# Performance work log

Measured on AMD Instinct MI355X. Metric: run time of the kernel, lower is better.

## Reference

```python
import jax, jax.numpy as jnp
import numpy as np

B, T, E, H = 2, 2048, 1024, 16
D = E // H  # head_dim = 64


def setup_inputs() -> dict:
    key = jax.random.key(0)
    ks = jax.random.split(key, 7)
    s = 1.0 / np.sqrt(E)
    queries = jax.random.normal(ks[0], (B, T, E), dtype=jnp.float32)
    keys = jax.random.normal(ks[1], (B, T, E), dtype=jnp.float32)
    values = jax.random.normal(ks[2], (B, T, E), dtype=jnp.float32)
    # causal mask: True where attention is disallowed (masked_fill semantics)
    mask = jnp.triu(jnp.ones((T, T), dtype=bool), k=1)[None, None]  # [1,1,T,T]
    Wq = jax.random.uniform(ks[3], (E, E), jnp.float32, -s, s)
    Wk = jax.random.uniform(ks[4], (E, E), jnp.float32, -s, s)
    Wv = jax.random.uniform(ks[5], (E, E), jnp.float32, -s, s)
    Wo = jax.random.uniform(ks[6], (E, E), jnp.float32, -s, s)
    return {"queries": queries, "keys": keys, "values": values, "mask": mask,
            "Wq": Wq, "Wk": Wk, "Wv": Wv, "Wo": Wo}


def _split(x):
    # [B,T,E] -> [B,H,T,D]
    return x.reshape(B, T, H, D).transpose(0, 2, 1, 3)


def reference(queries, keys, values, mask, Wq, Wk, Wv, Wo):
    # nn.Linear(E,E,bias=False): y = x @ W.T
    q = _split(queries @ Wq.T)  # [B,H,T,D]
    k = _split(keys @ Wk.T)
    v = _split(values @ Wv.T)
    scores = jnp.einsum('bhqd,bhkd->bhqk', q, k) / jnp.sqrt(jnp.float32(D))
    scores = jnp.where(mask, -jnp.inf, scores)
    weights = jax.nn.softmax(scores, axis=-1)
    attn = jnp.einsum('bhqk,bhkd->bhqd', weights, v)  # [B,H,T,D]
    joined = attn.transpose(0, 2, 1, 3).reshape(B, T, E)
    return joined @ Wo.T
```

## Files before the change

kernel.cpp:

```cpp
#include <hip/hip_runtime.h>
#include <hip/hip_bf16.h>

#define T_DIM 2048
#define E_DIM 1024
#define MM 4096
#define NN 1024
#define KK 1024
#define MSZ ((size_t)MM * KK)
#define WSZ ((size_t)NN * KK)

typedef __attribute__((ext_vector_type(8))) short bh8;
typedef __attribute__((ext_vector_type(4))) short bh4;
typedef __attribute__((ext_vector_type(4))) float fx4;

static __device__ __forceinline__ short f2bf(float f) {
  union { float f; unsigned u; } v; v.f = f;
  unsigned r = (v.u + 0x7fffu + ((v.u >> 16) & 1u)) >> 16;
  return (short)(unsigned short)r;
}

static __device__ __forceinline__ void gload16(const void* g, void* l) {
  __builtin_amdgcn_global_load_lds(
      (const __attribute__((address_space(1))) unsigned*)g,
      (__attribute__((address_space(3))) unsigned*)l, 16, 0, 0);
}

template<int CTRL>
static __device__ __forceinline__ float dppf(float x) {
  union { float f; int i; } a, b;
  a.f = x;
  b.i = __builtin_amdgcn_update_dpp(0, a.i, CTRL, 0xf, 0xf, false);
  return b.f;
}
static __device__ __forceinline__ float rowmax16(float x) {
  x = fmaxf(x, dppf<0x121>(x));
  x = fmaxf(x, dppf<0x122>(x));
  x = fmaxf(x, dppf<0x124>(x));
  x = fmaxf(x, dppf<0x128>(x));
  return x;
}
static __device__ __forceinline__ float rowsum16(float x) {
  x += dppf<0x121>(x);
  x += dppf<0x122>(x);
  x += dppf<0x124>(x);
  x += dppf<0x128>(x);
  return x;
}

__global__ __launch_bounds__(256) void cvt_w(const float* __restrict__ s0,
                                             const float* __restrict__ s1,
                                             const float* __restrict__ s2,
                                             const float* __restrict__ s3,
                                             short* __restrict__ dst) {
  int a = blockIdx.y;
  const float* sp = a == 0 ? s0 : a == 1 ? s1 : a == 2 ? s2 : s3;
  size_t i = ((size_t)blockIdx.x * 256 + threadIdx.x) * 8;
  fx4 x = *(const fx4*)(sp + i);
  fx4 y = *(const fx4*)(sp + i + 4);
  bh8 o;
#pragma unroll
  for (int j = 0; j < 4; j++) { o[j] = f2bf(x[j]); o[4 + j] = f2bf(y[j]); }
  *(bh8*)(dst + (size_t)a * WSZ + i) = o;
}

__global__ __launch_bounds__(256) void cvt_act(const float* __restrict__ s0,
                                               const float* __restrict__ s1,
                                               const float* __restrict__ s2,
                                               short* __restrict__ dst) {
  int a = blockIdx.y;
  const float* sp = a == 0 ? s0 : a == 1 ? s1 : s2;
  size_t i = ((size_t)blockIdx.x * 256 + threadIdx.x) * 8;
  fx4 x = *(const fx4*)(sp + i);
  fx4 y = *(const fx4*)(sp + i + 4);
  bh8 o;
#pragma unroll
  for (int j = 0; j < 4; j++) { o[j] = f2bf(x[j]); o[4 + j] = f2bf(y[j]); }
  *(bh8*)(dst + (size_t)a * MSZ + i) = o;
}

template<bool AF32, bool OUTF32>
__global__ __launch_bounds__(256) void gemm_fast(const void* __restrict__ A0,
                                                 const void* __restrict__ A1,
                                                 const void* __restrict__ A2,
                                                 const short* __restrict__ W0,
                                                 void* __restrict__ C0)
{
  __shared__ short As[128 * 32];
  __shared__ short Bs[128 * 32];
  const int tid = threadIdx.x;
  const int lane = tid & 63, w = tid >> 6;
  const int lm = lane & 15, lg = lane >> 4;
  const int wr = w >> 1, wc = w & 1;
  const int m0 = blockIdx.y * 128, n0 = blockIdx.x * 128;
  const int z = blockIdx.z;
  const void* Ap = z == 0 ? A0 : z == 1 ? A1 : A2;
  const short* W = W0 + (size_t)z * WSZ;

  fx4 acc[4][4] = {};

  for (int k0 = 0; k0 < KK; k0 += 32) {
    __syncthreads();
#pragma unroll
    for (int c = 0; c < 2; c++) {
      int idx = c * 256 + tid;
      int row = idx >> 2, kc = idx & 3;
      gload16(W + (size_t)(n0 + row) * KK + k0 + kc * 8, Bs + idx * 8);
      if constexpr (AF32) {
        const float* Af = (const float*)Ap;
        const float* src = Af + (size_t)(m0 + row) * KK + k0 + kc * 8;
        fx4 x = *(const fx4*)src;
        fx4 y = *(const fx4*)(src + 4);
        bh8 o;
#pragma unroll
        for (int j = 0; j < 4; j++) { o[j] = f2bf(x[j]); o[4 + j] = f2bf(y[j]); }
        *(bh8*)&As[idx * 8] = o;
      } else {
        const short* Ab = (const short*)Ap;
        gload16(Ab + (size_t)(m0 + row) * KK + k0 + kc * 8, As + idx * 8);
      }
    }
    __syncthreads();
    bh8 af[4], bf[4];
#pragma unroll
    for (int mi = 0; mi < 4; mi++)
      af[mi] = *(const bh8*)&As[(wr * 64 + mi * 16 + lm) * 32 + lg * 8];
#pragma unroll
    for (int ni = 0; ni < 4; ni++)
      bf[ni] = *(const bh8*)&Bs[(wc * 64 + ni * 16 + lm) * 32 + lg * 8];
#pragma unroll
    for (int mi = 0; mi < 4; mi++)
#pragma unroll
      for (int ni = 0; ni < 4; ni++)
        acc[mi][ni] = __builtin_amdgcn_mfma_f32_16x16x32_bf16(af[mi], bf[ni], acc[mi][ni], 0, 0, 0);
  }

#pragma unroll
  for (int mi = 0; mi < 4; mi++)
#pragma unroll
    for (int ni = 0; ni < 4; ni++) {
      int row = m0 + wr * 64 + mi * 16 + lg * 4;
      int col = n0 + wc * 64 + ni * 16 + lm;
#pragma unroll
      for (int r = 0; r < 4; r++) {
        float vv = acc[mi][ni][r];
        if constexpr (OUTF32) ((float*)C0)[(size_t)z * MSZ + (size_t)(row + r) * NN + col] = vv;
        else ((short*)C0)[(size_t)z * MSZ + (size_t)(row + r) * NN + col] = f2bf(vv);
      }
    }
}

__global__ __launch_bounds__(256) void gemm_out64(const short* __restrict__ A,
                                                  const short* __restrict__ W,
                                                  float* __restrict__ C)
{
  __shared__ short As[64 * 32];
  __shared__ short Bs[128 * 32];
  const int tid = threadIdx.x;
  const int lane = tid & 63, w = tid >> 6;
  const int lm = lane & 15, lg = lane >> 4;
  const int lin = blockIdx.x + 8 * blockIdx.y;
  const int swz = (lin & 7) * 64 + (lin >> 3);
  const int n0 = (swz & 7) * 128, m0 = (swz >> 3) * 64;

  fx4 acc[4][2] = {};

  for (int k0 = 0; k0 < KK; k0 += 32) {
    __syncthreads();
    {
      int row = tid >> 2, kc = tid & 3;
      gload16(A + (size_t)(m0 + row) * KK + k0 + kc * 8, As + tid * 8);
#pragma unroll
      for (int c = 0; c < 2; c++) {
        int idx = c * 256 + tid;
        int brow = idx >> 2, bkc = idx & 3;
        gload16(W + (size_t)(n0 + brow) * KK + k0 + bkc * 8, Bs + idx * 8);
      }
    }
    __syncthreads();
    bh8 af[4], bf[2];
#pragma unroll
    for (int mi = 0; mi < 4; mi++)
      af[mi] = *(const bh8*)&As[(mi * 16 + lm) * 32 + lg * 8];
#pragma unroll
    for (int ni = 0; ni < 2; ni++)
      bf[ni] = *(const bh8*)&Bs[(w * 32 + ni * 16 + lm) * 32 + lg * 8];
#pragma unroll
    for (int mi = 0; mi < 4; mi++)
#pragma unroll
      for (int ni = 0; ni < 2; ni++)
        acc[mi][ni] = __builtin_amdgcn_mfma_f32_16x16x32_bf16(af[mi], bf[ni], acc[mi][ni], 0, 0, 0);
  }

#pragma unroll
  for (int mi = 0; mi < 4; mi++)
#pragma unroll
    for (int ni = 0; ni < 2; ni++) {
      int row = m0 + mi * 16 + lg * 4;
      int col = n0 + w * 32 + ni * 16 + lm;
#pragma unroll
      for (int r = 0; r < 4; r++)
        C[(size_t)(row + r) * NN + col] = acc[mi][ni][r];
    }
}

template<bool AF32, bool OUTF32>
__global__ __launch_bounds__(256) void gemm_nt(const void* __restrict__ Ap,
                                               const float* __restrict__ Bw,
                                               void* __restrict__ Cp,
                                               int M, int N, int K)
{
  __shared__ short As[128 * 40];
  __shared__ short Bs[128 * 40];
  const int tid = threadIdx.x;
  const int lane = tid & 63;
  const int w = tid >> 6;
  const int lm = lane & 15;
  const int lg = lane >> 4;
  const int wr = w >> 1, wc = w & 1;
  const int m0 = blockIdx.y * 128, n0 = blockIdx.x * 128;

  fx4 acc[4][4] = {};

  for (int k0 = 0; k0 < K; k0 += 32) {
    __syncthreads();
#pragma unroll
    for (int i = 0; i < 4; ++i) {
      int g = i * 256 + tid;
      int row = g >> 3, cg = g & 7;
      bh4 a4;
      if constexpr (AF32) {
        const float* A = (const float*)Ap;
        fx4 v = *(const fx4*)(A + (size_t)(m0 + row) * K + k0 + cg * 4);
#pragma unroll
        for (int j = 0; j < 4; j++) a4[j] = f2bf(v[j]);
      } else {
        const short* A = (const short*)Ap;
        a4 = *(const bh4*)(A + (size_t)(m0 + row) * K + k0 + cg * 4);
      }
      *(bh4*)&As[row * 40 + cg * 4] = a4;

      fx4 bv = *(const fx4*)(Bw + (size_t)(n0 + row) * K + k0 + cg * 4);
      bh4 b4;
#pragma unroll
      for (int j = 0; j < 4; j++) b4[j] = f2bf(bv[j]);
      *(bh4*)&Bs[row * 40 + cg * 4] = b4;
    }
    __syncthreads();

    bh8 af[4], bf[4];
#pragma unroll
    for (int mi = 0; mi < 4; mi++)
      af[mi] = *(const bh8*)&As[(wr * 64 + mi * 16 + lm) * 40 + lg * 8];
#pragma unroll
    for (int ni = 0; ni < 4; ni++)
      bf[ni] = *(const bh8*)&Bs[(wc * 64 + ni * 16 + lm) * 40 + lg * 8];
#pragma unroll
    for (int mi = 0; mi < 4; mi++)
#pragma unroll
      for (int ni = 0; ni < 4; ni++)
        acc[mi][ni] = __builtin_amdgcn_mfma_f32_16x16x32_bf16(af[mi], bf[ni], acc[mi][ni], 0, 0, 0);
  }

#pragma unroll
  for (int mi = 0; mi < 4; mi++) {
#pragma unroll
    for (int ni = 0; ni < 4; ni++) {
      int row = m0 + wr * 64 + mi * 16 + lg * 4;
      int col = n0 + wc * 64 + ni * 16 + lm;
#pragma unroll
      for (int r = 0; r < 4; r++) {
        float vv = acc[mi][ni][r];
        if constexpr (OUTF32) ((float*)Cp)[(size_t)(row + r) * N + col] = vv;
        else        ((short*)Cp)[(size_t)(row + r) * N + col] = f2bf(vv);
      }
    }
  }
}

__global__ __launch_bounds__(256) void attn_kernel(const short* __restrict__ Q,
                                                   const short* __restrict__ Kb,
                                                   const short* __restrict__ Vb,
                                                   short* __restrict__ At)
{
  __shared__ short Kl[2][64 * 64];
  __shared__ short Vt[2][64 * 64];
  __shared__ short Pl[4 * 16 * 72];

  const int tid = threadIdx.x;
  const int lane = tid & 63;
  const int w = tid >> 6;
  const int lm = lane & 15;
  const int lg = lane >> 4;
  const int lin = blockIdx.x + 16 * blockIdx.y;
  const int swz = (lin & 7) * 64 + (lin >> 3);
  const int pi = swz & 15;
  const int bh = swz >> 4;
  const size_t headoff = (size_t)(bh >> 4) * T_DIM * E_DIM + (size_t)(bh & 15) * 64;

  const float SCALE2 = 0.125f * 1.44269504f;

  const int r0 = tid >> 3, ch0 = tid & 7;
  const int r1 = (256 + tid) >> 3, ch1 = tid & 7;

  for (int s = 0; s < 2; s++) {
    const int qt = s ? (31 - pi) : pi;
    const int q0 = qt * 64;

    const int qrow = q0 + w * 16 + lm;
    bh8 qf[2];
#pragma unroll
    for (int ks = 0; ks < 2; ks++)
      qf[ks] = *(const bh8*)(Q + headoff + (size_t)qrow * E_DIM + ks * 32 + lg * 8);

    fx4 oacc[4] = {};
    float m_r[4], l_r[4];
#pragma unroll
    for (int r = 0; r < 4; r++) { m_r[r] = -INFINITY; l_r[r] = 0.0f; }

    {
      gload16(Kb + headoff + (size_t)r0 * E_DIM + ((ch0 ^ (r0 & 7)) * 8), &Kl[0][tid * 8]);
      gload16(Kb + headoff + (size_t)r1 * E_DIM + ((ch1 ^ (r1 & 7)) * 8), &Kl[0][(256 + tid) * 8]);
      bh8 v8a = *(const bh8*)(Vb + headoff + (size_t)r0 * E_DIM + ch0 * 8);
      bh8 v8b = *(const bh8*)(Vb + headoff + (size_t)r1 * E_DIM + ch1 * 8);
#pragma unroll
      for (int j = 0; j < 8; j++) {
        int d = ch0 * 8 + j;
        Vt[0][d * 64 + (((r0 >> 3) ^ ((ch0 + j) & 7)) * 8) + (r0 & 7)] = v8a[j];
        Vt[0][d * 64 + (((r1 >> 3) ^ ((ch1 + j) & 7)) * 8) + (r1 & 7)] = v8b[j];
      }
    }
    __syncthreads();

    int cur = 0;
    for (int t = 0; t <= qt; ++t) {
      const bool pre = (t < qt);
      bh8 v8a, v8b;
      if (pre) {
        const int kvn = (t + 1) * 64;
        gload16(Kb + headoff + (size_t)(kvn + r0) * E_DIM + ((ch0 ^ (r0 & 7)) * 8),
                &Kl[cur ^ 1][tid * 8]);
        gload16(Kb + headoff + (size_t)(kvn + r1) * E_DIM + ((ch1 ^ (r1 & 7)) * 8),
                &Kl[cur ^ 1][(256 + tid) * 8]);
        v8a = *(const bh8*)(Vb + headoff + (size_t)(kvn + r0) * E_DIM + ch0 * 8);
        v8b = *(const bh8*)(Vb + headoff + (size_t)(kvn + r1) * E_DIM + ch1 * 8);
      }

      fx4 sacc[4] = {};
#pragma unroll
      for (int nb = 0; nb < 4; nb++) {
        const int rK = nb * 16 + lm;
#pragma unroll
        for (int ks = 0; ks < 2; ks++) {
          bh8 kf = *(const bh8*)&Kl[cur][rK * 64 + (((ks * 4 + lg) ^ (lm & 7)) * 8)];
          sacc[nb] = __builtin_amdgcn_mfma_f32_16x16x32_bf16(qf[ks], kf, sacc[nb], 0, 0, 0);
        }
      }

      float sv[4][4];
      const bool maskt = (t == qt);
#pragma unroll
      for (int nb = 0; nb < 4; nb++)
#pragma unroll
        for (int r = 0; r < 4; r++) {
          float x = sacc[nb][r] * SCALE2;
          if (maskt && (nb * 16 + lm > w * 16 + lg * 4 + r)) x = -INFINITY;
          sv[nb][r] = x;
        }

      float p[4][4];
#pragma unroll
      for (int r = 0; r < 4; r++) {
        float rm = fmaxf(fmaxf(sv[0][r], sv[1][r]), fmaxf(sv[2][r], sv[3][r]));
        rm = rowmax16(rm);
        float mn = fmaxf(m_r[r], rm);
        float fac = exp2f(m_r[r] - mn);
        float ps = 0.0f;
#pragma unroll
        for (int nb = 0; nb < 4; nb++) { p[nb][r] = exp2f(sv[nb][r] - mn); ps += p[nb][r]; }
        ps = rowsum16(ps);
        l_r[r] = l_r[r] * fac + ps;
        m_r[r] = mn;
#pragma unroll
        for (int db = 0; db < 4; db++) oacc[db][r] *= fac;
      }

#pragma unroll
      for (int nb = 0; nb < 4; nb++)
#pragma unroll
        for (int r = 0; r < 4; r++)
          Pl[w * 1152 + (lg * 4 + r) * 72 + nb * 16 + lm] = f2bf(p[nb][r]);

      bh8 pa[2];
#pragma unroll
      for (int ks = 0; ks < 2; ks++)
        pa[ks] = *(const bh8*)&Pl[w * 1152 + lm * 72 + ks * 32 + lg * 8];
#pragma unroll
      for (int db = 0; db < 4; db++) {
        const int d = db * 16 + lm;
        const int gsw = ((d >> 3) + (d & 7)) & 7;
#pragma unroll
        for (int ks = 0; ks < 2; ks++) {
          bh8 vf = *(const bh8*)&Vt[cur][d * 64 + (((ks * 4 + lg) ^ gsw) * 8)];
          oacc[db] = __builtin_amdgcn_mfma_f32_16x16x32_bf16(pa[ks], vf, oacc[db], 0, 0, 0);
        }
      }

      if (pre) {
#pragma unroll
        for (int j = 0; j < 8; j++) {
          int d = ch0 * 8 + j;
          Vt[cur ^ 1][d * 64 + (((r0 >> 3) ^ ((ch0 + j) & 7)) * 8) + (r0 & 7)] = v8a[j];
          Vt[cur ^ 1][d * 64 + (((r1 >> 3) ^ ((ch1 + j) & 7)) * 8) + (r1 & 7)] = v8b[j];
        }
      }
      __syncthreads();
      cur ^= 1;
    }

#pragma unroll
    for (int r = 0; r < 4; r++) {
      float rl = 1.0f / l_r[r];
      int row = q0 + w * 16 + lg * 4 + r;
#pragma unroll
      for (int db = 0; db < 4; db++)
        At[headoff + (size_t)row * E_DIM + db * 16 + lm] = f2bf(oacc[db][r] * rl);
    }
  }
}

extern "C" void kernel_launch(void* const* d_in, const int* in_sizes, int n_in,
                              void* d_out, int out_size, void* d_ws, size_t ws_size,
                              hipStream_t stream)
{
  const float* q  = (const float*)d_in[0];
  const float* k  = (const float*)d_in[1];
  const float* v  = (const float*)d_in[2];
  const float* Wq = (const float*)d_in[4];
  const float* Wk = (const float*)d_in[5];
  const float* Wv = (const float*)d_in[6];
  const float* Wo = (const float*)d_in[7];

  short* Qb  = (short*)d_ws;
  short* Kbb = Qb + MSZ;
  short* Vbb = Kbb + MSZ;
  short* wqb = Vbb + MSZ;
  short* Xq  = wqb + 4 * WSZ;
  short* At  = Xq;

  const size_t need_full = (3 * MSZ + 4 * WSZ + 3 * MSZ) * 2;
  const size_t need_mid  = (4 * MSZ + 4 * WSZ) * 2;

  if (ws_size >= need_full) {
    cvt_act<<<dim3(MSZ / (256 * 8), 3), 256, 0, stream>>>(q, k, v, Xq);
    cvt_w<<<dim3(WSZ / (256 * 8), 4), 256, 0, stream>>>(Wq, Wk, Wv, Wo, wqb);
    gemm_fast<false, false><<<dim3(NN / 128, MM / 128, 3), 256, 0, stream>>>(
        Xq, Xq + MSZ, Xq + 2 * MSZ, wqb, Qb);
    attn_kernel<<<dim3(16, 32), 256, 0, stream>>>(Qb, Kbb, Vbb, At);
    gemm_out64<<<dim3(NN / 128, MM / 64), 256, 0, stream>>>(
        At, wqb + 3 * WSZ, (float*)d_out);
  } else if (ws_size >= need_mid) {
    short* At2  = Vbb + MSZ;
    short* wqb2 = At2 + MSZ;
    cvt_w<<<dim3(WSZ / (256 * 8), 4), 256, 0, stream>>>(Wq, Wk, Wv, Wo, wqb2);
    gemm_fast<true, false><<<dim3(NN / 128, MM / 128, 3), 256, 0, stream>>>(q, k, v, wqb2, Qb);
    attn_kernel<<<dim3(16, 32), 256, 0, stream>>>(Qb, Kbb, Vbb, At2);
    gemm_out64<<<dim3(NN / 128, MM / 64), 256, 0, stream>>>(
        At2, wqb2 + 3 * WSZ, (float*)d_out);
  } else {
    short* At2 = Vbb + MSZ;
    dim3 gg(NN / 128, MM / 128);
    gemm_nt<true, false><<<gg, 256, 0, stream>>>(q, Wq, Qb, MM, NN, KK);
    gemm_nt<true, false><<<gg, 256, 0, stream>>>(k, Wk, Kbb, MM, NN, KK);
    gemm_nt<true, false><<<gg, 256, 0, stream>>>(v, Wv, Vbb, MM, NN, KK);
    attn_kernel<<<dim3(16, 32), 256, 0, stream>>>(Qb, Kbb, Vbb, At2);
    gemm_nt<false, true><<<gg, 256, 0, stream>>>(At2, Wo, d_out, MM, NN, KK);
  }
}
```

Measured before the change: 251.5 us.

## Fold softmax scale into Wq, use hardware bf16 pack, deepen GEMM K-step, skip rescale

Multiplies Wq by the softmax scale times log2(e) during weight conversion, so the attention kernel no longer scales scores. Float-to-bf16 rounding now uses the packed v_cvt_pk_bf16_f32 instruction instead of integer arithmetic. Both GEMMs load 64 K-elements per barrier pair instead of 32, which halves the number of sync rounds. The attention kernel skips the running-max rescale of the accumulators when no row max grew across the wave. The code path for mid-sized workspaces is removed. Rounding of Q moves slightly because the scale is now applied before the bf16 cast.

```diff
diff --git a/kernel.cpp b/kernel.cpp
--- a/kernel.cpp
+++ b/kernel.cpp
@@ -12,11 +12,19 @@
 typedef __attribute__((ext_vector_type(8))) short bh8;
 typedef __attribute__((ext_vector_type(4))) short bh4;
 typedef __attribute__((ext_vector_type(4))) float fx4;
+typedef __attribute__((ext_vector_type(4))) unsigned ux4;
+
+#define QSCALE 0.18033688f
 
 static __device__ __forceinline__ short f2bf(float f) {
-  union { float f; unsigned u; } v; v.f = f;
-  unsigned r = (v.u + 0x7fffu + ((v.u >> 16) & 1u)) >> 16;
-  return (short)(unsigned short)r;
+  unsigned o;
+  asm("v_cvt_pk_bf16_f32 %0, %1, %1" : "=v"(o) : "v"(f));
+  return (short)(o & 0xffffu);
+}
+static __device__ __forceinline__ unsigned f2bf2(float lo, float hi) {
+  unsigned o;
+  asm("v_cvt_pk_bf16_f32 %0, %1, %2" : "=v"(o) : "v"(lo), "v"(hi));
+  return o;
 }
 
 static __device__ __forceinline__ void gload16(const void* g, void* l) {
@@ -54,13 +62,16 @@
                                              short* __restrict__ dst) {
   int a = blockIdx.y;
   const float* sp = a == 0 ? s0 : a == 1 ? s1 : a == 2 ? s2 : s3;
+  const float sc = (a == 0) ? QSCALE : 1.0f;
   size_t i = ((size_t)blockIdx.x * 256 + threadIdx.x) * 8;
   fx4 x = *(const fx4*)(sp + i);
   fx4 y = *(const fx4*)(sp + i + 4);
-  bh8 o;
-#pragma unroll
-  for (int j = 0; j < 4; j++) { o[j] = f2bf(x[j]); o[4 + j] = f2bf(y[j]); }
-  *(bh8*)(dst + (size_t)a * WSZ + i) = o;
+  ux4 o;
+  o[0] = f2bf2(x[0] * sc, x[1] * sc);
+  o[1] = f2bf2(x[2] * sc, x[3] * sc);
+  o[2] = f2bf2(y[0] * sc, y[1] * sc);
+  o[3] = f2bf2(y[2] * sc, y[3] * sc);
+  *(ux4*)(dst + (size_t)a * WSZ + i) = o;
 }
 
 __global__ __launch_bounds__(256) void cvt_act(const float* __restrict__ s0,
@@ -72,66 +83,65 @@
   size_t i = ((size_t)blockIdx.x * 256 + threadIdx.x) * 8;
   fx4 x = *(const fx4*)(sp + i);
   fx4 y = *(const fx4*)(sp + i + 4);
-  bh8 o;
-#pragma unroll
-  for (int j = 0; j < 4; j++) { o[j] = f2bf(x[j]); o[4 + j] = f2bf(y[j]); }
-  *(bh8*)(dst + (size_t)a * MSZ + i) = o;
-}
-
-template<bool AF32, bool OUTF32>
-__global__ __launch_bounds__(256) void gemm_fast(const void* __restrict__ A0,
-                                                 const void* __restrict__ A1,
-                                                 const void* __restrict__ A2,
+  ux4 o;
+  o[0] = f2bf2(x[0], x[1]);
+  o[1] = f2bf2(x[2], x[3]);
+  o[2] = f2bf2(y[0], y[1]);
+  o[3] = f2bf2(y[2], y[3]);
+  *(ux4*)(dst + (size_t)a * MSZ + i) = o;
+}
+
+template<bool OUTF32>
+__global__ __launch_bounds__(256) void gemm_fast(const short* __restrict__ A0,
+                                                 const short* __restrict__ A1,
+                                                 const short* __restrict__ A2,
                                                  const short* __restrict__ W0,
                                                  void* __restrict__ C0)
 {
-  __shared__ short As[128 * 32];
-  __shared__ short Bs[128 * 32];
+  __shared__ short As[2][128 * 32];
+  __shared__ short Bs[2][128 * 32];
   const int tid = threadIdx.x;
   const int lane = tid & 63, w = tid >> 6;
   const int lm = lane & 15, lg = lane >> 4;
   const int wr = w >> 1, wc = w & 1;
   const int m0 = blockIdx.y * 128, n0 = blockIdx.x * 128;
   const int z = blockIdx.z;
-  const void* Ap = z == 0 ? A0 : z == 1 ? A1 : A2;
+  const short* Ab = z == 0 ? A0 : z == 1 ? A1 : A2;
   const short* W = W0 + (size_t)z * WSZ;
 
   fx4 acc[4][4] = {};
 
-  for (int k0 = 0; k0 < KK; k0 += 32) {
-    __syncthreads();
-#pragma unroll
-    for (int c = 0; c < 2; c++) {
-      int idx = c * 256 + tid;
-      int row = idx >> 2, kc = idx & 3;
-      gload16(W + (size_t)(n0 + row) * KK + k0 + kc * 8, Bs + idx * 8);
-      if constexpr (AF32) {
-        const float* Af = (const float*)Ap;
-        const float* src = Af + (size_t)(m0 + row) * KK + k0 + kc * 8;
-        fx4 x = *(const fx4*)src;
-        fx4 y = *(const fx4*)(src + 4);
-        bh8 o;
-#pragma unroll
-        for (int j = 0; j < 4; j++) { o[j] = f2bf(x[j]); o[4 + j] = f2bf(y[j]); }
-        *(bh8*)&As[idx * 8] = o;
-      } else {
-        const short* Ab = (const short*)Ap;
-        gload16(Ab + (size_t)(m0 + row) * KK + k0 + kc * 8, As + idx * 8);
-      }
-    }
-    __syncthreads();
-    bh8 af[4], bf[4];
+  for (int k0 = 0; k0 < KK; k0 += 64) {
+    __syncthreads();
+#pragma unroll
+    for (int h = 0; h < 2; h++) {
+#pragma unroll
+      for (int c = 0; c < 2; c++) {
+        int idx = c * 256 + tid;
+        int row = idx >> 2, kc = idx & 3;
+        gload16(W + (size_t)(n0 + row) * KK + k0 + h * 32 + kc * 8, &Bs[h][idx * 8]);
+        gload16(Ab + (size_t)(m0 + row) * KK + k0 + h * 32 + kc * 8, &As[h][idx * 8]);
+      }
+    }
+    __syncthreads();
+    bh8 af[4][2], bf[4][2];
 #pragma unroll
     for (int mi = 0; mi < 4; mi++)
-      af[mi] = *(const bh8*)&As[(wr * 64 + mi * 16 + lm) * 32 + lg * 8];
+#pragma unroll
+      for (int h = 0; h < 2; h++)
+        af[mi][h] = *(const bh8*)&As[h][(wr * 64 + mi * 16 + lm) * 32 + lg * 8];
 #pragma unroll
     for (int ni = 0; ni < 4; ni++)
-      bf[ni] = *(const bh8*)&Bs[(wc * 64 + ni * 16 + lm) * 32 + lg * 8];
+#pragma unroll
+      for (int h = 0; h < 2; h++)
+        bf[ni][h] = *(const bh8*)&Bs[h][(wc * 64 + ni * 16 + lm) * 32 + lg * 8];
 #pragma unroll
     for (int mi = 0; mi < 4; mi++)
 #pragma unroll
       for (int ni = 0; ni < 4; ni++)
-        acc[mi][ni] = __builtin_amdgcn_mfma_f32_16x16x32_bf16(af[mi], bf[ni], acc[mi][ni], 0, 0, 0);
+#pragma unroll
+        for (int h = 0; h < 2; h++)
+          acc[mi][ni] = __builtin_amdgcn_mfma_f32_16x16x32_bf16(af[mi][h], bf[ni][h], acc[mi][ni], 0, 0, 0);
   }
 
 #pragma unroll
@@ -153,8 +163,8 @@
                                                   const short* __restrict__ W,
                                                   float* __restrict__ C)
 {
-  __shared__ short As[64 * 32];
-  __shared__ short Bs[128 * 32];
+  __shared__ short As[2][64 * 32];
+  __shared__ short Bs[2][128 * 32];
   const int tid = threadIdx.x;
   const int lane = tid & 63, w = tid >> 6;
   const int lm = lane & 15, lg = lane >> 4;
@@ -164,31 +174,40 @@
 
   fx4 acc[4][2] = {};
 
-  for (int k0 = 0; k0 < KK; k0 += 32) {
-    __syncthreads();
-    {
-      int row = tid >> 2, kc = tid & 3;
-      gload16(A + (size_t)(m0 + row) * KK + k0 + kc * 8, As + tid * 8);
+  for (int k0 = 0; k0 < KK; k0 += 64) {
+    __syncthreads();
+#pragma unroll
+    for (int h = 0; h < 2; h++) {
+      {
+        int row = tid >> 2, kc = tid & 3;
+        gload16(A + (size_t)(m0 + row) * KK + k0 + h * 32 + kc * 8, &As[h][tid * 8]);
+      }
 #pragma unroll
       for (int c = 0; c < 2; c++) {
         int idx = c * 256 + tid;
         int brow = idx >> 2, bkc = idx & 3;
-        gload16(W + (size_t)(n0 + brow) * KK + k0 + bkc * 8, Bs + idx * 8);
-      }
-    }
-    __syncthreads();
-    bh8 af[4], bf[2];
+        gload16(W + (size_t)(n0 + brow) * KK + k0 + h * 32 + bkc * 8, &Bs[h][idx * 8]);
+      }
+    }
+    __syncthreads();
+    bh8 af[4][2], bf[2][2];
 #pragma unroll
     for (int mi = 0; mi < 4; mi++)
-      af[mi] = *(const bh8*)&As[(mi * 16 + lm) * 32 + lg * 8];
+#pragma unroll
+      for (int h = 0; h < 2; h++)
+        af[mi][h] = *(const bh8*)&As[h][(mi * 16 + lm) * 32 + lg * 8];
 #pragma unroll
     for (int ni = 0; ni < 2; ni++)
-      bf[ni] = *(const bh8*)&Bs[(w * 32 + ni * 16 + lm) * 32 + lg * 8];
+#pragma unroll
+      for (int h = 0; h < 2; h++)
+        bf[ni][h] = *(const bh8*)&Bs[h][(w * 32 + ni * 16 + lm) * 32 + lg * 8];
 #pragma unroll
     for (int mi = 0; mi < 4; mi++)
 #pragma unroll
       for (int ni = 0; ni < 2; ni++)
-        acc[mi][ni] = __builtin_amdgcn_mfma_f32_16x16x32_bf16(af[mi], bf[ni], acc[mi][ni], 0, 0, 0);
+#pragma unroll
+        for (int h = 0; h < 2; h++)
+          acc[mi][ni] = __builtin_amdgcn_mfma_f32_16x16x32_bf16(af[mi][h], bf[ni][h], acc[mi][ni], 0, 0, 0);
   }
 
 #pragma unroll
@@ -277,6 +296,7 @@
   }
 }
 
+template<bool PRESCALED>
 __global__ __launch_bounds__(256) void attn_kernel(const short* __restrict__ Q,
                                                    const short* __restrict__ Kb,
                                                    const short* __restrict__ Vb,
@@ -297,7 +317,7 @@
   const int bh = swz >> 4;
   const size_t headoff = (size_t)(bh >> 4) * T_DIM * E_DIM + (size_t)(bh & 15) * 64;
 
-  const float SCALE2 = 0.125f * 1.44269504f;
+  const float SCALE2 = QSCALE;
 
   const int r0 = tid >> 3, ch0 = tid & 7;
   const int r1 = (256 + tid) >> 3, ch1 = tid & 7;
@@ -362,26 +382,39 @@
       for (int nb = 0; nb < 4; nb++)
 #pragma unroll
         for (int r = 0; r < 4; r++) {
-          float x = sacc[nb][r] * SCALE2;
+          float x = PRESCALED ? sacc[nb][r] : sacc[nb][r] * SCALE2;
           if (maskt && (nb * 16 + lm > w * 16 + lg * 4 + r)) x = -INFINITY;
           sv[nb][r] = x;
         }
 
-      float p[4][4];
+      float rm4[4];
+      bool stable = true;
 #pragma unroll
       for (int r = 0; r < 4; r++) {
         float rm = fmaxf(fmaxf(sv[0][r], sv[1][r]), fmaxf(sv[2][r], sv[3][r]));
         rm = rowmax16(rm);
-        float mn = fmaxf(m_r[r], rm);
-        float fac = exp2f(m_r[r] - mn);
+        rm4[r] = rm;
+        stable = stable && (rm <= m_r[r]);
+      }
+      if (!__all(stable)) {
+#pragma unroll
+        for (int r = 0; r < 4; r++) {
+          float mn = fmaxf(m_r[r], rm4[r]);
+          float fac = exp2f(m_r[r] - mn);
+          l_r[r] *= fac;
+          m_r[r] = mn;
+#pragma unroll
+          for (int db = 0; db < 4; db++) oacc[db][r] *= fac;
+        }
+      }
+      float p[4][4];
+#pragma unroll
+      for (int r = 0; r < 4; r++) {
         float ps = 0.0f;
 #pragma unroll
-        for (int nb = 0; nb < 4; nb++) { p[nb][r] = exp2f(sv[nb][r] - mn); ps += p[nb][r]; }
+        for (int nb = 0; nb < 4; nb++) { p[nb][r] = exp2f(sv[nb][r] - m_r[r]); ps += p[nb][r]; }
         ps = rowsum16(ps);
-        l_r[r] = l_r[r] * fac + ps;
-        m_r[r] = mn;
-#pragma unroll
-        for (int db = 0; db < 4; db++) oacc[db][r] *= fac;
+        l_r[r] += ps;
       }
 
 #pragma unroll
@@ -448,31 +481,22 @@
   short* At  = Xq;
 
   const size_t need_full = (3 * MSZ + 4 * WSZ + 3 * MSZ) * 2;
-  const size_t need_mid  = (4 * MSZ + 4 * WSZ) * 2;
 
   if (ws_size >= need_full) {
     cvt_act<<<dim3(MSZ / (256 * 8), 3), 256, 0, stream>>>(q, k, v, Xq);
     cvt_w<<<dim3(WSZ / (256 * 8), 4), 256, 0, stream>>>(Wq, Wk, Wv, Wo, wqb);
-    gemm_fast<false, false><<<dim3(NN / 128, MM / 128, 3), 256, 0, stream>>>(
+    gemm_fast<false><<<dim3(NN / 128, MM / 128, 3), 256, 0, stream>>>(
         Xq, Xq + MSZ, Xq + 2 * MSZ, wqb, Qb);
-    attn_kernel<<<dim3(16, 32), 256, 0, stream>>>(Qb, Kbb, Vbb, At);
+    attn_kernel<true><<<dim3(16, 32), 256, 0, stream>>>(Qb, Kbb, Vbb, At);
     gemm_out64<<<dim3(NN / 128, MM / 64), 256, 0, stream>>>(
         At, wqb + 3 * WSZ, (float*)d_out);
-  } else if (ws_size >= need_mid) {
-    short* At2  = Vbb + MSZ;
-    short* wqb2 = At2 + MSZ;
-    cvt_w<<<dim3(WSZ / (256 * 8), 4), 256, 0, stream>>>(Wq, Wk, Wv, Wo, wqb2);
-    gemm_fast<true, false><<<dim3(NN / 128, MM / 128, 3), 256, 0, stream>>>(q, k, v, wqb2, Qb);
-    attn_kernel<<<dim3(16, 32), 256, 0, stream>>>(Qb, Kbb, Vbb, At2);
-    gemm_out64<<<dim3(NN / 128, MM / 64), 256, 0, stream>>>(
-        At2, wqb2 + 3 * WSZ, (float*)d_out);
   } else {
     short* At2 = Vbb + MSZ;
     dim3 gg(NN / 128, MM / 128);
     gemm_nt<true, false><<<gg, 256, 0, stream>>>(q, Wq, Qb, MM, NN, KK);
     gemm_nt<true, false><<<gg, 256, 0, stream>>>(k, Wk, Kbb, MM, NN, KK);
     gemm_nt<true, false><<<gg, 256, 0, stream>>>(v, Wv, Vbb, MM, NN, KK);
-    attn_kernel<<<dim3(16, 32), 256, 0, stream>>>(Qb, Kbb, Vbb, At2);
+    attn_kernel<false><<<dim3(16, 32), 256, 0, stream>>>(Qb, Kbb, Vbb, At2);
     gemm_nt<false, true><<<gg, 256, 0, stream>>>(At2, Wo, d_out, MM, NN, KK);
   }
 }
```

Measured after the change: 260.0 us. 3.4% more time.
